# Performance work log

Hardware: AMD Instinct MI355X
Metric: run time of the kernel (lower is better)

The kernel has to match this reference:

```python
import jax, jax.numpy as jnp
import numpy as np

B, H, W, C = 4, 64, 64, 256
CQ = C // 8


def setup_inputs() -> dict:
    key = jax.random.key(0)
    ks = jax.random.split(key, 5)
    scale = 0.02
    inputs = jax.random.normal(ks[0], (B, H, W, C), dtype=jnp.float32)
    wq = jax.random.normal(ks[1], (C, CQ), dtype=jnp.float32) * scale
    bq = jnp.zeros((CQ,), dtype=jnp.float32)
    wk = jax.random.normal(ks[2], (C, CQ), dtype=jnp.float32) * scale
    bk = jnp.zeros((CQ,), dtype=jnp.float32)
    wv = jax.random.normal(ks[3], (C, C), dtype=jnp.float32) * scale
    bv = jnp.zeros((C,), dtype=jnp.float32)
    gamma = jax.random.normal(ks[4], (), dtype=jnp.float32)
    return {"inputs": inputs, "wq": wq, "bq": bq, "wk": wk, "bk": bk,
            "wv": wv, "bv": bv, "gamma": gamma}


def reference(inputs, wq, bq, wk, bk, wv, bv, gamma):
    b, h, w, c = inputs.shape
    n = h * w
    x = inputs.reshape(b, n, c)  # [B, N, C]
    # 1x1 convs == per-pixel linear projections
    q = x @ wq + bq              # [B, N, Cq]
    k = x @ wk + bk              # [B, N, Cq]
    v = x @ wv + bv              # [B, N, C]
    # energy = Q K^T (no sqrt scaling, as in the original)
    energy = jnp.einsum('bnd,bmd->bnm', q, k)      # [B, N, N]
    attention = jax.nn.softmax(energy, axis=-1)    # softmax over keys
    # x_out = V^T @ attention^T -> per query: sum_m attn[n,m] * v[m]
    x_out = jnp.einsum('bnm,bmc->bnc', attention, v)  # [B, N, C]
    x_out = x_out.reshape(b, h, w, c)
    return gamma * x_out + inputs
```

## Files before the change

### kernel.cpp

```cpp
#include <hip/hip_runtime.h>
#include <hip/hip_bf16.h>

typedef __attribute__((ext_vector_type(8))) short bf16x8;
typedef __attribute__((ext_vector_type(4))) float f32x4;
typedef __attribute__((ext_vector_type(4))) int int4v;

#define NB 4
#define NN 4096
#define NC 256
#define NSPLIT 4
#define KEYS_PER_SPLIT 1024
#define KT_ITERS 16

__device__ __forceinline__ unsigned short f2bf(float f) {
    unsigned u = __builtin_bit_cast(unsigned, f);
    u += 0x7fffu + ((u >> 16) & 1u);
    return (unsigned short)(u >> 16);
}
__device__ __forceinline__ float bf2f(unsigned short u) {
    unsigned v = ((unsigned)u) << 16;
    return __builtin_bit_cast(float, v);
}
__device__ __forceinline__ void load_lds16(const void* g, void* l) {
    __builtin_amdgcn_global_load_lds(
        (const __attribute__((address_space(1))) void*)g,
        (__attribute__((address_space(3))) void*)l, 16, 0, 0);
}

__global__ __launch_bounds__(256) void wt_kernel(
    const float* __restrict__ wq, const float* __restrict__ wk,
    const float* __restrict__ wv, unsigned short* __restrict__ wt)
{
    const int c = blockIdx.x;
    const int k = threadIdx.x;
    float v;
    if (c < 32)      v = wq[k * 32 + c];
    else if (c < 64) v = wk[k * 32 + (c - 32)];
    else             v = wv[k * 256 + (c - 64)];
    wt[c * 256 + k] = f2bf(v);
}

__global__ __launch_bounds__(256) void proj_kernel(
    const float* __restrict__ x,
    const unsigned short* __restrict__ wt,
    const float* __restrict__ bq, const float* __restrict__ bk,
    const float* __restrict__ bv,
    unsigned short* __restrict__ q_ws,
    unsigned short* __restrict__ k_ws,
    unsigned short* __restrict__ vt_ws)
{
    const int lane = threadIdx.x & 63;
    const int w    = threadIdx.x >> 6;
    const int l15  = lane & 15, hh = lane >> 4;
    const int m0   = blockIdx.x * 16;
    const int ct0  = w * 5;

    f32x4 acc[5];
    #pragma unroll
    for (int i = 0; i < 5; ++i) acc[i] = f32x4{0.f, 0.f, 0.f, 0.f};

    const float* xrow = x + (size_t)(m0 + l15) * 256 + hh * 8;
    #pragma unroll
    for (int ks = 0; ks < 8; ++ks) {
        float4 xa = ((const float4*)(xrow + ks * 32))[0];
        float4 xb = ((const float4*)(xrow + ks * 32))[1];
        bf16x8 afrag;
        afrag[0] = (short)f2bf(xa.x); afrag[1] = (short)f2bf(xa.y);
        afrag[2] = (short)f2bf(xa.z); afrag[3] = (short)f2bf(xa.w);
        afrag[4] = (short)f2bf(xb.x); afrag[5] = (short)f2bf(xb.y);
        afrag[6] = (short)f2bf(xb.z); afrag[7] = (short)f2bf(xb.w);
        #pragma unroll
        for (int c = 0; c < 5; ++c) {
            bf16x8 bfrag = *(const bf16x8*)(wt + (size_t)((ct0 + c) * 16 + l15) * 256 + ks * 32 + hh * 8);
            acc[c] = __builtin_amdgcn_mfma_f32_16x16x32_bf16(afrag, bfrag, acc[c], 0, 0, 0);
        }
    }

    const int b    = m0 >> 12;
    const int nloc = m0 & 4095;
    #pragma unroll
    for (int c = 0; c < 5; ++c) {
        const int ct = ct0 + c;
        const int c0 = ct * 16;
        float bias;
        if (c0 < 32)      bias = bq[c0 + l15];
        else if (c0 < 64) bias = bk[c0 - 32 + l15];
        else              bias = bv[c0 - 64 + l15];
        if (c0 < 64) {
            unsigned short* dst = (c0 < 32) ? q_ws : k_ws;
            const int cc = (c0 < 32) ? c0 : (c0 - 32);
            #pragma unroll
            for (int i = 0; i < 4; ++i)
                dst[(size_t)(m0 + hh * 4 + i) * 32 + cc + l15] = f2bf(acc[c][i] + bias);
        } else {
            const int cc = c0 - 64 + l15;
            #pragma unroll
            for (int i = 0; i < 4; i += 2) {
                unsigned lo = f2bf(acc[c][i]     + bias);
                unsigned hi = f2bf(acc[c][i + 1] + bias);
                *(unsigned*)(vt_ws + ((size_t)b * 256 + cc) * 4096 + nloc + hh * 4 + i)
                    = lo | (hi << 16);
            }
        }
    }
}

__global__ __launch_bounds__(512, 4) void attn_kernel(
    const unsigned short* __restrict__ q_ws,
    const unsigned short* __restrict__ k_ws,
    const unsigned short* __restrict__ vt_ws,
    unsigned short* __restrict__ opart,
    float* __restrict__ lpart)
{
    __shared__ unsigned short vt_lds[256 * 64];
    __shared__ unsigned short p_lds[128 * 64];

    const int lane = threadIdx.x & 63;
    const int wid  = threadIdx.x >> 6;
    const int l15  = lane & 15, hh = lane >> 4;

    const int xcd   = blockIdx.x & 7;
    const int j     = blockIdx.x >> 3;
    const int combo = xcd * 2 + (j >> 5);
    const int qtile = j & 31;
    const int split = combo >> 2;
    const int b     = combo & 3;
    const int q0    = qtile * 128;
    const int key0  = split * KEYS_PER_SPLIT;

    const int wr   = wid >> 2;
    const int kc   = wid & 3;

    bf16x8 aq[4];
    #pragma unroll
    for (int qt = 0; qt < 4; ++qt)
        aq[qt] = *(const bf16x8*)(q_ws + (size_t)(b * 4096 + q0 + wr * 64 + qt * 16 + l15) * 32 + hh * 8);

    f32x4 acc[4][4];
    float lsum[4][4];
    #pragma unroll
    for (int qt = 0; qt < 4; ++qt) {
        #pragma unroll
        for (int ct = 0; ct < 4; ++ct) acc[qt][ct] = f32x4{0.f, 0.f, 0.f, 0.f};
        #pragma unroll
        for (int i = 0; i < 4; ++i) lsum[qt][i] = 0.f;
    }

    const unsigned short* vt_base = vt_ws + (size_t)b * 256 * 4096;
    const unsigned short* k_base  = k_ws + (size_t)b * 4096 * 32;

    for (int kt = 0; kt < KT_ITERS; ++kt) {
        const int kb = key0 + kt * 64;
        __syncthreads();

        #pragma unroll
        for (int e = 0; e < 4; ++e) {
            int idx  = e * 512 + threadIdx.x;
            int c    = idx >> 3;
            int slot = idx & 7;
            const unsigned short* src = vt_base + (size_t)c * 4096 + kb + ((slot ^ (c & 7)) << 3);
            load_lds16(src, (char*)vt_lds + idx * 16);
        }

        bf16x8 bkf = *(const bf16x8*)(k_base + (size_t)(kb + kc * 16 + l15) * 32 + hh * 8);
        f32x4 e2[4];
        #pragma unroll
        for (int qt = 0; qt < 4; ++qt) {
            f32x4 z = {0.f, 0.f, 0.f, 0.f};
            e2[qt] = __builtin_amdgcn_mfma_f32_16x16x32_bf16(aq[qt], bkf, z, 0, 0, 0);
        }

        #pragma unroll
        for (int qt = 0; qt < 4; ++qt) {
            #pragma unroll
            for (int i = 0; i < 4; ++i) {
                float p = __expf(e2[qt][i]);
                lsum[qt][i] += p;
                int r   = wr * 64 + qt * 16 + hh * 4 + i;
                int off = kc * 32 + l15 * 2;
                int sw  = (((off >> 4) ^ (r & 7)) << 4) | (off & 15);
                *(unsigned short*)((char*)p_lds + r * 128 + sw) = f2bf(p);
            }
        }
        __syncthreads();

        __builtin_amdgcn_s_setprio(1);
        #pragma unroll
        for (int s = 0; s < 2; ++s) {
            bf16x8 ap[4];
            #pragma unroll
            for (int qt = 0; qt < 4; ++qt) {
                int r = wr * 64 + qt * 16 + l15;
                ap[qt] = *(const bf16x8*)((char*)p_lds + r * 128 + (((s * 4 + hh) ^ (r & 7)) << 4));
            }
            #pragma unroll
            for (int ct = 0; ct < 4; ++ct) {
                int c = kc * 64 + ct * 16 + l15;
                bf16x8 bvf = *(const bf16x8*)((char*)vt_lds + c * 128 + (((s * 4 + hh) ^ (c & 7)) << 4));
                #pragma unroll
                for (int qt = 0; qt < 4; ++qt)
                    acc[qt][ct] = __builtin_amdgcn_mfma_f32_16x16x32_bf16(ap[qt], bvf, acc[qt][ct], 0, 0, 0);
            }
        }
        __builtin_amdgcn_s_setprio(0);
    }

    __syncthreads();
    float* l_s = (float*)p_lds;
    #pragma unroll
    for (int qt = 0; qt < 4; ++qt) {
        #pragma unroll
        for (int i = 0; i < 4; ++i) {
            float s = lsum[qt][i];
            s += __shfl_xor(s, 1); s += __shfl_xor(s, 2);
            s += __shfl_xor(s, 4); s += __shfl_xor(s, 8);
            if (l15 == 0) l_s[kc * 128 + wr * 64 + qt * 16 + hh * 4 + i] = s;
        }
    }
    __syncthreads();

    const size_t rowbase = (size_t)(split * 4 + b) * 4096 + q0 + wr * 64;
    if (kc == 0 && l15 == 0) {
        #pragma unroll
        for (int qt = 0; qt < 4; ++qt) {
            #pragma unroll
            for (int i = 0; i < 4; ++i) {
                int row = wr * 64 + qt * 16 + hh * 4 + i;
                lpart[rowbase + qt * 16 + hh * 4 + i] =
                    l_s[row] + l_s[128 + row] + l_s[256 + row] + l_s[384 + row];
            }
        }
    }

    #pragma unroll
    for (int qt = 0; qt < 4; ++qt) {
        #pragma unroll
        for (int i = 0; i < 4; ++i) {
            int r = qt * 16 + hh * 4 + i;
            #pragma unroll
            for (int ct = 0; ct < 4; ++ct) {
                int c = kc * 64 + ct * 16 + l15;
                opart[(rowbase + r) * 256 + c] = f2bf(acc[qt][ct][i]);
            }
        }
    }
}

__global__ __launch_bounds__(256) void combine_kernel(
    const unsigned short* __restrict__ opart,
    const float* __restrict__ lpart,
    const float* __restrict__ x,
    const float* __restrict__ gamma_p,
    float* __restrict__ out)
{
    const int t  = blockIdx.x * 256 + threadIdx.x;
    const int r  = t >> 5;
    const int c0 = (t & 31) * 8;
    const float gamma = gamma_p[0];

    float sumO[8];
    #pragma unroll
    for (int j = 0; j < 8; ++j) sumO[j] = 0.f;
    float suml = 0.f;
    #pragma unroll
    for (int s = 0; s < NSPLIT; ++s) {
        bf16x8 o = *(const bf16x8*)(opart + ((size_t)(s * 16384 + r)) * 256 + c0);
        #pragma unroll
        for (int j = 0; j < 8; ++j) sumO[j] += bf2f((unsigned short)o[j]);
        suml += lpart[s * 16384 + r];
    }
    const float inv = gamma / suml;
    const size_t base = (size_t)r * 256 + c0;
    float4 x0 = *(const float4*)(x + base);
    float4 x1 = *(const float4*)(x + base + 4);
    float4 o0, o1;
    o0.x = sumO[0] * inv + x0.x; o0.y = sumO[1] * inv + x0.y;
    o0.z = sumO[2] * inv + x0.z; o0.w = sumO[3] * inv + x0.w;
    o1.x = sumO[4] * inv + x1.x; o1.y = sumO[5] * inv + x1.y;
    o1.z = sumO[6] * inv + x1.z; o1.w = sumO[7] * inv + x1.w;
    *(float4*)(out + base)     = o0;
    *(float4*)(out + base + 4) = o1;
}

extern "C" void kernel_launch(void* const* d_in, const int* in_sizes, int n_in,
                              void* d_out, int out_size, void* d_ws, size_t ws_size,
                              hipStream_t stream) {
    const float* x     = (const float*)d_in[0];
    const float* wq    = (const float*)d_in[1];
    const float* bq    = (const float*)d_in[2];
    const float* wk    = (const float*)d_in[3];
    const float* bk    = (const float*)d_in[4];
    const float* wv    = (const float*)d_in[5];
    const float* bv    = (const float*)d_in[6];
    const float* gamma = (const float*)d_in[7];
    float* out = (float*)d_out;

    char* ws = (char*)d_ws;
    unsigned short* wt    = (unsigned short*)(ws);
    unsigned short* q_ws  = (unsigned short*)(ws + 163840);
    unsigned short* k_ws  = (unsigned short*)(ws + 1212416);
    unsigned short* vt_ws = (unsigned short*)(ws + 2260992);
    unsigned short* opart = (unsigned short*)(ws + 10649600);
    float*          lpart = (float*)(ws + 44204032);

    wt_kernel     <<<320,  256, 0, stream>>>(wq, wk, wv, wt);
    proj_kernel   <<<1024, 256, 0, stream>>>(x, wt, bq, bk, bv, q_ws, k_ws, vt_ws);
    attn_kernel   <<<512,  512, 0, stream>>>(q_ws, k_ws, vt_ws, opart, lpart);
    combine_kernel<<<2048, 256, 0, stream>>>(opart, lpart, x, gamma, out);
}
```

Measured before the change: 121.0 us.

## Switch attention to 32x32 MFMA and keep probabilities in registers

```diff
diff --git a/kernel.cpp b/kernel.cpp
--- a/kernel.cpp
+++ b/kernel.cpp
@@ -3,6 +3,7 @@
 
 typedef __attribute__((ext_vector_type(8))) short bf16x8;
 typedef __attribute__((ext_vector_type(4))) float f32x4;
+typedef __attribute__((ext_vector_type(16))) float f32x16;
 typedef __attribute__((ext_vector_type(4))) int int4v;
 
 #define NB 4
@@ -25,6 +26,14 @@
     __builtin_amdgcn_global_load_lds(
         (const __attribute__((address_space(1))) void*)g,
         (__attribute__((address_space(3))) void*)l, 16, 0, 0);
+}
+__device__ __forceinline__ unsigned cvtpk(float lo, float hi) {
+    unsigned d;
+    asm("v_cvt_pk_bf16_f32 %0, %1, %2" : "=v"(d) : "v"(lo), "v"(hi));
+    return d;
+}
+__device__ __forceinline__ void pl32swap(unsigned &a, unsigned &b) {
+    asm volatile("v_permlane32_swap_b32 %0, %1" : "+v"(a), "+v"(b));
 }
 
 __global__ __launch_bounds__(256) void wt_kernel(
@@ -105,7 +114,7 @@
     }
 }
 
-__global__ __launch_bounds__(512, 4) void attn_kernel(
+__global__ __launch_bounds__(256, 2) void attn_kernel(
     const unsigned short* __restrict__ q_ws,
     const unsigned short* __restrict__ k_ws,
     const unsigned short* __restrict__ vt_ws,
@@ -113,11 +122,13 @@
     float* __restrict__ lpart)
 {
     __shared__ unsigned short vt_lds[256 * 64];
-    __shared__ unsigned short p_lds[128 * 64];
 
     const int lane = threadIdx.x & 63;
     const int wid  = threadIdx.x >> 6;
-    const int l15  = lane & 15, hh = lane >> 4;
+    const int l31  = lane & 31;
+    const int hi   = lane >> 5;
+    const int wr   = wid >> 1;
+    const int wc   = wid & 1;
 
     const int xcd   = blockIdx.x & 7;
     const int j     = blockIdx.x >> 3;
@@ -128,23 +139,22 @@
     const int q0    = qtile * 128;
     const int key0  = split * KEYS_PER_SPLIT;
 
-    const int wr   = wid >> 2;
-    const int kc   = wid & 3;
-
-    bf16x8 aq[4];
-    #pragma unroll
-    for (int qt = 0; qt < 4; ++qt)
-        aq[qt] = *(const bf16x8*)(q_ws + (size_t)(b * 4096 + q0 + wr * 64 + qt * 16 + l15) * 32 + hh * 8);
-
-    f32x4 acc[4][4];
-    float lsum[4][4];
-    #pragma unroll
-    for (int qt = 0; qt < 4; ++qt) {
-        #pragma unroll
-        for (int ct = 0; ct < 4; ++ct) acc[qt][ct] = f32x4{0.f, 0.f, 0.f, 0.f};
-        #pragma unroll
-        for (int i = 0; i < 4; ++i) lsum[qt][i] = 0.f;
-    }
+    bf16x8 aq[2][2];
+    #pragma unroll
+    for (int qt = 0; qt < 2; ++qt)
+        #pragma unroll
+        for (int cs = 0; cs < 2; ++cs)
+            aq[qt][cs] = *(const bf16x8*)(q_ws +
+                (size_t)(b * 4096 + q0 + wr * 64 + qt * 32 + l31) * 32 + cs * 16 + hi * 8);
+
+    f32x16 acc[2][4];
+    #pragma unroll
+    for (int qt = 0; qt < 2; ++qt)
+        #pragma unroll
+        for (int ct = 0; ct < 4; ++ct)
+            #pragma unroll
+            for (int r = 0; r < 16; ++r) acc[qt][ct][r] = 0.f;
+    float lsum[2] = {0.f, 0.f};
 
     const unsigned short* vt_base = vt_ws + (size_t)b * 256 * 4096;
     const unsigned short* k_base  = k_ws + (size_t)b * 4096 * 32;
@@ -154,94 +164,123 @@
         __syncthreads();
 
         #pragma unroll
-        for (int e = 0; e < 4; ++e) {
-            int idx  = e * 512 + threadIdx.x;
+        for (int e = 0; e < 8; ++e) {
+            int idx  = e * 256 + threadIdx.x;
             int c    = idx >> 3;
             int slot = idx & 7;
             const unsigned short* src = vt_base + (size_t)c * 4096 + kb + ((slot ^ (c & 7)) << 3);
             load_lds16(src, (char*)vt_lds + idx * 16);
         }
 
-        bf16x8 bkf = *(const bf16x8*)(k_base + (size_t)(kb + kc * 16 + l15) * 32 + hh * 8);
-        f32x4 e2[4];
-        #pragma unroll
-        for (int qt = 0; qt < 4; ++qt) {
-            f32x4 z = {0.f, 0.f, 0.f, 0.f};
-            e2[qt] = __builtin_amdgcn_mfma_f32_16x16x32_bf16(aq[qt], bkf, z, 0, 0, 0);
-        }
-
-        #pragma unroll
-        for (int qt = 0; qt < 4; ++qt) {
-            #pragma unroll
-            for (int i = 0; i < 4; ++i) {
-                float p = __expf(e2[qt][i]);
-                lsum[qt][i] += p;
-                int r   = wr * 64 + qt * 16 + hh * 4 + i;
-                int off = kc * 32 + l15 * 2;
-                int sw  = (((off >> 4) ^ (r & 7)) << 4) | (off & 15);
-                *(unsigned short*)((char*)p_lds + r * 128 + sw) = f2bf(p);
+        bf16x8 ak[2][2];
+        #pragma unroll
+        for (int ktile = 0; ktile < 2; ++ktile)
+            #pragma unroll
+            for (int cs = 0; cs < 2; ++cs)
+                ak[ktile][cs] = *(const bf16x8*)(k_base +
+                    (size_t)(kb + ktile * 32 + l31) * 32 + cs * 16 + hi * 8);
+
+        unsigned pa[2][4][4];
+        #pragma unroll
+        for (int qt = 0; qt < 2; ++qt) {
+            f32x16 zed;
+            #pragma unroll
+            for (int r = 0; r < 16; ++r) zed[r] = 0.f;
+            f32x16 e0 = __builtin_amdgcn_mfma_f32_32x32x16_bf16(ak[0][0], aq[qt][0], zed, 0, 0, 0);
+            e0 = __builtin_amdgcn_mfma_f32_32x32x16_bf16(ak[0][1], aq[qt][1], e0, 0, 0, 0);
+            f32x16 e1 = __builtin_amdgcn_mfma_f32_32x32x16_bf16(ak[1][0], aq[qt][0], zed, 0, 0, 0);
+            e1 = __builtin_amdgcn_mfma_f32_32x32x16_bf16(ak[1][1], aq[qt][1], e1, 0, 0, 0);
+
+            float s = 0.f;
+            #pragma unroll
+            for (int t2 = 0; t2 < 2; ++t2) {
+                #pragma unroll
+                for (int h = 0; h < 2; ++h) {
+                    float p0, p1, p2, p3, p4, p5, p6, p7;
+                    if (t2 == 0) {
+                        p0 = __expf(e0[h*8+0]); p1 = __expf(e0[h*8+1]);
+                        p2 = __expf(e0[h*8+2]); p3 = __expf(e0[h*8+3]);
+                        p4 = __expf(e0[h*8+4]); p5 = __expf(e0[h*8+5]);
+                        p6 = __expf(e0[h*8+6]); p7 = __expf(e0[h*8+7]);
+                    } else {
+                        p0 = __expf(e1[h*8+0]); p1 = __expf(e1[h*8+1]);
+                        p2 = __expf(e1[h*8+2]); p3 = __expf(e1[h*8+3]);
+                        p4 = __expf(e1[h*8+4]); p5 = __expf(e1[h*8+5]);
+                        p6 = __expf(e1[h*8+6]); p7 = __expf(e1[h*8+7]);
+                    }
+                    s += ((p0 + p1) + (p2 + p3)) + ((p4 + p5) + (p6 + p7));
+                    unsigned d0 = cvtpk(p0, p1);
+                    unsigned d1 = cvtpk(p2, p3);
+                    unsigned d2 = cvtpk(p4, p5);
+                    unsigned d3 = cvtpk(p6, p7);
+                    pl32swap(d0, d2);
+                    pl32swap(d1, d3);
+                    const int ks = t2 * 2 + h;
+                    pa[qt][ks][0] = d0; pa[qt][ks][1] = d1;
+                    pa[qt][ks][2] = d2; pa[qt][ks][3] = d3;
+                }
             }
+            lsum[qt] += s;
         }
         __syncthreads();
 
         __builtin_amdgcn_s_setprio(1);
         #pragma unroll
-        for (int s = 0; s < 2; ++s) {
-            bf16x8 ap[4];
-            #pragma unroll
-            for (int qt = 0; qt < 4; ++qt) {
-                int r = wr * 64 + qt * 16 + l15;
-                ap[qt] = *(const bf16x8*)((char*)p_lds + r * 128 + (((s * 4 + hh) ^ (r & 7)) << 4));
+        for (int ks = 0; ks < 4; ++ks) {
+            #pragma unroll
+            for (int ct = 0; ct < 4; ++ct) {
+                int c = wc * 128 + ct * 32 + l31;
+                int chunk = ks * 2 + hi;
+                bf16x8 bvf = *(const bf16x8*)((char*)vt_lds + c * 128 + ((chunk ^ (c & 7)) << 4));
+                #pragma unroll
+                for (int qt = 0; qt < 2; ++qt) {
+                    union { unsigned u[4]; bf16x8 v; } cvt;
+                    cvt.u[0] = pa[qt][ks][0]; cvt.u[1] = pa[qt][ks][1];
+                    cvt.u[2] = pa[qt][ks][2]; cvt.u[3] = pa[qt][ks][3];
+                    acc[qt][ct] = __builtin_amdgcn_mfma_f32_32x32x16_bf16(cvt.v, bvf, acc[qt][ct], 0, 0, 0);
+                }
             }
-            #pragma unroll
-            for (int ct = 0; ct < 4; ++ct) {
-                int c = kc * 64 + ct * 16 + l15;
-                bf16x8 bvf = *(const bf16x8*)((char*)vt_lds + c * 128 + (((s * 4 + hh) ^ (c & 7)) << 4));
+        }
+        __builtin_amdgcn_s_setprio(0);
+    }
+
+    #pragma unroll
+    for (int qt = 0; qt < 2; ++qt)
+        lsum[qt] += __shfl_xor(lsum[qt], 32);
+
+    const size_t rowb = (size_t)(split * 4 + b) * 4096 + q0;
+    if (wc == 0 && hi == 0) {
+        #pragma unroll
+        for (int qt = 0; qt < 2; ++qt)
+            lpart[rowb + wr * 64 + qt * 32 + l31] = lsum[qt];
+    }
+
+    #pragma unroll
+    for (int h = 0; h < 2; ++h) {
+        __syncthreads();
+        if (wr == h) {
+            #pragma unroll
+            for (int qt = 0; qt < 2; ++qt) {
                 #pragma unroll
-                for (int qt = 0; qt < 4; ++qt)
-                    acc[qt][ct] = __builtin_amdgcn_mfma_f32_16x16x32_bf16(ap[qt], bvf, acc[qt][ct], 0, 0, 0);
+                for (int ct = 0; ct < 4; ++ct) {
+                    #pragma unroll
+                    for (int rr = 0; rr < 16; ++rr) {
+                        int lr  = qt * 32 + (rr & 3) + 8 * (rr >> 2) + 4 * hi;
+                        int col = wc * 128 + ct * 32 + l31;
+                        int a   = lr * 512 + (((col >> 3) ^ (lr & 31)) << 4) + (col & 7) * 2;
+                        *(unsigned short*)((char*)vt_lds + a) = f2bf(acc[qt][ct][rr]);
+                    }
+                }
             }
         }
-        __builtin_amdgcn_s_setprio(0);
-    }
-
-    __syncthreads();
-    float* l_s = (float*)p_lds;
-    #pragma unroll
-    for (int qt = 0; qt < 4; ++qt) {
-        #pragma unroll
-        for (int i = 0; i < 4; ++i) {
-            float s = lsum[qt][i];
-            s += __shfl_xor(s, 1); s += __shfl_xor(s, 2);
-            s += __shfl_xor(s, 4); s += __shfl_xor(s, 8);
-            if (l15 == 0) l_s[kc * 128 + wr * 64 + qt * 16 + hh * 4 + i] = s;
-        }
-    }
-    __syncthreads();
-
-    const size_t rowbase = (size_t)(split * 4 + b) * 4096 + q0 + wr * 64;
-    if (kc == 0 && l15 == 0) {
-        #pragma unroll
-        for (int qt = 0; qt < 4; ++qt) {
-            #pragma unroll
-            for (int i = 0; i < 4; ++i) {
-                int row = wr * 64 + qt * 16 + hh * 4 + i;
-                lpart[rowbase + qt * 16 + hh * 4 + i] =
-                    l_s[row] + l_s[128 + row] + l_s[256 + row] + l_s[384 + row];
-            }
-        }
-    }
-
-    #pragma unroll
-    for (int qt = 0; qt < 4; ++qt) {
-        #pragma unroll
-        for (int i = 0; i < 4; ++i) {
-            int r = qt * 16 + hh * 4 + i;
-            #pragma unroll
-            for (int ct = 0; ct < 4; ++ct) {
-                int c = kc * 64 + ct * 16 + l15;
-                opart[(rowbase + r) * 256 + c] = f2bf(acc[qt][ct][i]);
-            }
+        __syncthreads();
+        #pragma unroll
+        for (int e = 0; e < 8; ++e) {
+            int g  = e * 256 + threadIdx.x;
+            int lr = g >> 5;
+            int sl = g & 31;
+            int4v v = *(const int4v*)((char*)vt_lds + lr * 512 + (((sl ^ (lr & 31)) << 4)));
+            *(int4v*)(opart + (rowb + h * 64 + lr) * 256 + sl * 8) = v;
         }
     }
 }
@@ -305,6 +344,6 @@
 
     wt_kernel     <<<320,  256, 0, stream>>>(wq, wk, wv, wt);
     proj_kernel   <<<1024, 256, 0, stream>>>(x, wt, bq, bk, bv, q_ws, k_ws, vt_ws);
-    attn_kernel   <<<512,  512, 0, stream>>>(q_ws, k_ws, vt_ws, opart, lpart);
+    attn_kernel   <<<512,  256, 0, stream>>>(q_ws, k_ws, vt_ws, opart, lpart);
     combine_kernel<<<2048, 256, 0, stream>>>(opart, lpart, x, gamma, out);
 }
```

New measurement: 147.1 us. 1.22x slower.
